# Performance work log

Measured on AMD Instinct MI355X. Metric: run time of the kernel, lower is better.

The kernel has to match this reference:

```python
import jax, jax.numpy as jnp
import numpy as np
import math

D_MODEL = 1024
D_HIDDEN = 64
H = 16
B = 2
N = 2048


def softmax_one(x, axis=-1):
    # exp(x - max) / (1 + sum(exp(x - max))) -- matches the torch code exactly
    m = jnp.max(x, axis=axis, keepdims=True)
    e = jnp.exp(x - m)
    return e / (1.0 + jnp.sum(e, axis=axis, keepdims=True))


def setup_inputs() -> dict:
    key = jax.random.key(0)
    ks = jax.random.split(key, 8)
    queries = jax.random.normal(ks[0], (B, N, D_MODEL), dtype=jnp.float32)
    keys = jax.random.normal(ks[1], (B, N, D_MODEL), dtype=jnp.float32)
    values = jax.random.normal(ks[2], (B, N, D_MODEL), dtype=jnp.float32)
    std = 0.02
    Wq = std * jax.random.normal(ks[3], (H * D_HIDDEN, D_MODEL), dtype=jnp.float32)
    Wk = std * jax.random.normal(ks[4], (H * D_HIDDEN, D_MODEL), dtype=jnp.float32)
    Wv = std * jax.random.normal(ks[5], (H * D_HIDDEN, D_MODEL), dtype=jnp.float32)
    Wo = std * jax.random.normal(ks[6], (D_MODEL, H * D_HIDDEN), dtype=jnp.float32)
    bq = jnp.zeros((H * D_HIDDEN,), jnp.float32)
    bk = jnp.zeros((H * D_HIDDEN,), jnp.float32)
    bv = jnp.zeros((H * D_HIDDEN,), jnp.float32)
    bo = jnp.zeros((D_MODEL,), jnp.float32)
    return {"queries": queries, "keys": keys, "values": values,
            "Wq": Wq, "bq": bq, "Wk": Wk, "bk": bk,
            "Wv": Wv, "bv": bv, "Wo": Wo, "bo": bo}


def reference(queries, keys, values, Wq, bq, Wk, bk, Wv, bv, Wo, bo):
    b_s, nq, _ = queries.shape
    nk = keys.shape[1]
    # projections: (b, n, h*dh) -> (b, h, n, dh)
    q = (queries @ Wq.T + bq).reshape(b_s, nq, H, D_HIDDEN).transpose(0, 2, 1, 3)
    k = (keys @ Wk.T + bk).reshape(b_s, nk, H, D_HIDDEN).transpose(0, 2, 1, 3)
    v = (values @ Wv.T + bv).reshape(b_s, nk, H, D_HIDDEN).transpose(0, 2, 1, 3)
    scale = 1.0 / math.sqrt(D_HIDDEN)
    scores = jnp.einsum('bhqd,bhkd->bhqk', q, k) * scale  # (b, h, nq, nk)
    attn = softmax_one(scores, axis=-1)  # dropout disabled (eval)
    out = jnp.einsum('bhqk,bhkd->bhqd', attn, v)  # (b, h, nq, dh)
    out = out.transpose(0, 2, 1, 3).reshape(b_s, nq, H * D_HIDDEN)
    out = out @ Wo.T + bo
    present = jnp.stack((k, v))  # (2, b, h, nk, dh)
    return (out, present)
```

## Files before the change

kernel.cpp:

```cpp
#include <hip/hip_runtime.h>
#include <math.h>

#define D_MODEL 1024
#define DH 64
#define NH 16
#define BS 2
#define SEQ 2048
#define MTOT (BS*SEQ)

typedef _Float16 f16x8 __attribute__((ext_vector_type(8)));
typedef _Float16 f16x4 __attribute__((ext_vector_type(4)));
typedef float f32x4 __attribute__((ext_vector_type(4)));
typedef unsigned int u32;

__device__ __forceinline__ void load_lds16(const void* g, void* l) {
    __builtin_amdgcn_global_load_lds(
        (const __attribute__((address_space(1))) u32*)g,
        (__attribute__((address_space(3))) u32*)l, 16, 0, 0);
}

__global__ __launch_bounds__(256) void convert_all_kernel(
    const float* __restrict__ s0, const float* __restrict__ s1, const float* __restrict__ s2,
    const float* __restrict__ s3, const float* __restrict__ s4, const float* __restrict__ s5,
    const float* __restrict__ s6,
    _Float16* __restrict__ d0, _Float16* __restrict__ d1, _Float16* __restrict__ d2,
    _Float16* __restrict__ d3, _Float16* __restrict__ d4, _Float16* __restrict__ d5,
    _Float16* __restrict__ d6, int nX, int nW)
{
    int y = blockIdx.y;
    const float* s; _Float16* d; int n;
    switch (y) {
        case 0: s = s0; d = d0; n = nX; break;
        case 1: s = s1; d = d1; n = nX; break;
        case 2: s = s2; d = d2; n = nX; break;
        case 3: s = s3; d = d3; n = nW; break;
        case 4: s = s4; d = d4; n = nW; break;
        case 5: s = s5; d = d5; n = nW; break;
        default: s = s6; d = d6; n = nW; break;
    }
    int i = (blockIdx.x * 256 + threadIdx.x) * 8;
    if (i < n) {
        float4 a = *(const float4*)(s + i);
        float4 b = *(const float4*)(s + i + 4);
        f16x8 o;
        o[0] = (_Float16)a.x; o[1] = (_Float16)a.y; o[2] = (_Float16)a.z; o[3] = (_Float16)a.w;
        o[4] = (_Float16)b.x; o[5] = (_Float16)b.y; o[6] = (_Float16)b.z; o[7] = (_Float16)b.w;
        *(f16x8*)(d + i) = o;
    }
}

__global__ __launch_bounds__(256) void qkv_proj_kernel(
    const _Float16* __restrict__ Xq, const _Float16* __restrict__ Xk, const _Float16* __restrict__ Xv,
    const _Float16* __restrict__ Wq, const _Float16* __restrict__ Wk, const _Float16* __restrict__ Wv,
    const float* __restrict__ bq, const float* __restrict__ bk, const float* __restrict__ bv,
    _Float16* __restrict__ qh, _Float16* __restrict__ kh, _Float16* __restrict__ vt,
    float* __restrict__ outp)
{
    __shared__ __align__(16) _Float16 ldsA[128][32];
    __shared__ __align__(16) _Float16 ldsB[128][32];

    const int jb = blockIdx.x >> 5;
    const int ib = blockIdx.x & 31;
    const int id = jb >> 3;
    const int col0 = (jb & 7) << 7;
    const int row0 = ib << 7;

    const _Float16* X  = (id == 0) ? Xq : (id == 1) ? Xk : Xv;
    const _Float16* W  = (id == 0) ? Wq : (id == 1) ? Wk : Wv;
    const float* bias  = (id == 0) ? bq : (id == 1) ? bk : bv;

    const int tid = threadIdx.x;
    const int w = tid >> 6, lane = tid & 63;
    const int quad = lane >> 4, l16 = lane & 15;
    const int wm = (w >> 1) << 6, wn = (w & 1) << 6;

    const int srow = w * 16 + (lane >> 2);
    const int scol = (lane & 3) << 3;

    const f32x4 zero = {0.f, 0.f, 0.f, 0.f};
    f32x4 acc[4][4];
#pragma unroll
    for (int i = 0; i < 4; i++)
#pragma unroll
        for (int j = 0; j < 4; j++) acc[i][j] = zero;

    for (int k0 = 0; k0 < D_MODEL; k0 += 32) {
        __syncthreads();
#pragma unroll
        for (int i = 0; i < 2; i++) {
            int r = i * 64 + srow;
            load_lds16(X + (size_t)(row0 + r) * D_MODEL + k0 + scol, &ldsA[i * 64 + w * 16][0]);
            load_lds16(W + (size_t)(col0 + r) * D_MODEL + k0 + scol, &ldsB[i * 64 + w * 16][0]);
        }
        __syncthreads();
        f16x8 af[4], bfr[4];
#pragma unroll
        for (int mi = 0; mi < 4; mi++) af[mi]  = *(const f16x8*)&ldsA[wm + mi*16 + l16][quad*8];
#pragma unroll
        for (int ni = 0; ni < 4; ni++) bfr[ni] = *(const f16x8*)&ldsB[wn + ni*16 + l16][quad*8];
#pragma unroll
        for (int mi = 0; mi < 4; mi++)
#pragma unroll
            for (int ni = 0; ni < 4; ni++)
                acc[mi][ni] = __builtin_amdgcn_mfma_f32_16x16x32_f16(af[mi], bfr[ni], acc[mi][ni], 0, 0, 0);
    }

    const size_t OUT0 = (size_t)MTOT * D_MODEL;
    const size_t PRES = (size_t)BS * NH * SEQ * DH;
#pragma unroll
    for (int ni = 0; ni < 4; ni++) {
        int gn = col0 + wn + ni * 16 + l16;
        float bias_v = bias[gn];
        int h = gn >> 6, d = gn & 63;
#pragma unroll
        for (int mi = 0; mi < 4; mi++) {
#pragma unroll
            for (int r = 0; r < 4; r++) {
                int gm = row0 + wm + mi * 16 + quad * 4 + r;
                float val = acc[mi][ni][r] + bias_v;
                int b = gm >> 11, n = gm & 2047;
                size_t bh = (size_t)(b * NH + h);
                size_t idx = (bh * SEQ + n) * DH + d;
                if (id == 0) {
                    qh[idx] = (_Float16)val;
                } else if (id == 1) {
                    outp[OUT0 + idx] = val;
                    kh[idx] = (_Float16)val;
                } else {
                    outp[OUT0 + PRES + idx] = val;
                    vt[(bh * DH + d) * SEQ + n] = (_Float16)val;
                }
            }
        }
    }
}

__global__ __launch_bounds__(256) void attn_kernel(
    const _Float16* __restrict__ qh, const _Float16* __restrict__ kh,
    const _Float16* __restrict__ vt, _Float16* __restrict__ aout)
{
    __shared__ __align__(16) _Float16 Kt[2][64][76];
    __shared__ __align__(16) _Float16 Vt[2][64][76];

    const int bh = blockIdx.x & 31;
    const int qt = blockIdx.x >> 5;
    const int b = bh >> 4, h = bh & 15;
    const int tid = threadIdx.x;
    const int w = tid >> 6, lane = tid & 63;
    const int quad = lane >> 4, l16 = lane & 15;
    const int qr0 = qt * 64 + w * 16;

    const _Float16* Qb = qh + (size_t)bh * SEQ * DH;
    const _Float16* Kb = kh + (size_t)bh * SEQ * DH;
    const _Float16* Vb = vt + (size_t)bh * DH * SEQ;

    const float QSCALE = 0.125f * 1.44269504f;
    f16x8 aq[2];
#pragma unroll
    for (int ks = 0; ks < 2; ks++) {
        f16x8 t = *(const f16x8*)(Qb + (size_t)(qr0 + l16) * DH + ks * 32 + quad * 8);
#pragma unroll
        for (int j = 0; j < 8; j++) t[j] = (_Float16)((float)t[j] * QSCALE);
        aq[ks] = t;
    }

    const int sr0 = tid >> 3, sc = (tid & 7) << 3;
    const int sr1 = sr0 + 32;

    {
        *(f16x8*)&Kt[0][sr0][sc] = *(const f16x8*)(Kb + (size_t)sr0 * DH + sc);
        *(f16x8*)&Kt[0][sr1][sc] = *(const f16x8*)(Kb + (size_t)sr1 * DH + sc);
        *(f16x8*)&Vt[0][sr0][sc] = *(const f16x8*)(Vb + (size_t)sr0 * SEQ + sc);
        *(f16x8*)&Vt[0][sr1][sc] = *(const f16x8*)(Vb + (size_t)sr1 * SEQ + sc);
    }
    __syncthreads();

    float m2 = -INFINITY, lsum = 0.f;
    const f32x4 zero = {0.f, 0.f, 0.f, 0.f};
    f32x4 accO[4];
#pragma unroll
    for (int db = 0; db < 4; db++) accO[db] = zero;

    for (int t = 0; t < SEQ / 64; t++) {
        const int cur = t & 1;
        const int kc = t * 64;

        f16x8 kr0, kr1, vr0, vr1;
        if (t + 1 < SEQ / 64) {
            const _Float16* kp = Kb + (size_t)(kc + 64) * DH;
            const _Float16* vp = Vb + kc + 64;
            kr0 = *(const f16x8*)(kp + (size_t)sr0 * DH + sc);
            kr1 = *(const f16x8*)(kp + (size_t)sr1 * DH + sc);
            vr0 = *(const f16x8*)(vp + (size_t)sr0 * SEQ + sc);
            vr1 = *(const f16x8*)(vp + (size_t)sr1 * SEQ + sc);
        }

        f32x4 sT[4];
#pragma unroll
        for (int nb = 0; nb < 4; nb++) sT[nb] = zero;
#pragma unroll
        for (int ks = 0; ks < 2; ks++)
#pragma unroll
            for (int nb = 0; nb < 4; nb++) {
                f16x8 kf = *(const f16x8*)&Kt[cur][nb*16 + l16][ks*32 + quad*8];
                sT[nb] = __builtin_amdgcn_mfma_f32_16x16x32_f16(kf, aq[ks], sT[nb], 0, 0, 0);
            }

        float smax = -INFINITY;
#pragma unroll
        for (int nb = 0; nb < 4; nb++)
#pragma unroll
            for (int r = 0; r < 4; r++) smax = fmaxf(smax, sT[nb][r]);
        smax = fmaxf(smax, __shfl_xor(smax, 16));
        smax = fmaxf(smax, __shfl_xor(smax, 32));
        float m2new = fmaxf(m2, smax);
        float alpha = __builtin_amdgcn_exp2f(m2 - m2new);

        float tsum = 0.f;
#pragma unroll
        for (int nb = 0; nb < 4; nb++)
#pragma unroll
            for (int r = 0; r < 4; r++) {
                float e = __builtin_amdgcn_exp2f(sT[nb][r] - m2new);
                sT[nb][r] = e;
                tsum += e;
            }
        tsum += __shfl_xor(tsum, 16);
        tsum += __shfl_xor(tsum, 32);
        lsum = lsum * alpha + tsum;
        m2 = m2new;

#pragma unroll
        for (int db = 0; db < 4; db++)
#pragma unroll
            for (int r = 0; r < 4; r++) accO[db][r] *= alpha;

        f16x4 pf[4];
#pragma unroll
        for (int nb = 0; nb < 4; nb++)
#pragma unroll
            for (int r = 0; r < 4; r++) pf[nb][r] = (_Float16)sT[nb][r];

#pragma unroll
        for (int db = 0; db < 4; db++)
#pragma unroll
            for (int nb = 0; nb < 4; nb++) {
                f16x4 vf = *(const f16x4*)&Vt[cur][db*16 + l16][nb*16 + quad*4];
                accO[db] = __builtin_amdgcn_mfma_f32_16x16x16f16(vf, pf[nb], accO[db], 0, 0, 0);
            }

        if (t + 1 < SEQ / 64) {
            *(f16x8*)&Kt[cur ^ 1][sr0][sc] = kr0;
            *(f16x8*)&Kt[cur ^ 1][sr1][sc] = kr1;
            *(f16x8*)&Vt[cur ^ 1][sr0][sc] = vr0;
            *(f16x8*)&Vt[cur ^ 1][sr1][sc] = vr1;
        }
        __syncthreads();
    }

    const float inv = 1.f / (1.f + lsum);
    const int q = qr0 + l16;
    _Float16* orow = aout + ((size_t)b * SEQ + q) * D_MODEL + h * DH + quad * 4;
#pragma unroll
    for (int db = 0; db < 4; db++) {
        f16x4 o;
#pragma unroll
        for (int r = 0; r < 4; r++) o[r] = (_Float16)(accO[db][r] * inv);
        *(f16x4*)(orow + db * 16) = o;
    }
}

__global__ __launch_bounds__(256) void out_proj_kernel(
    const _Float16* __restrict__ aout, const _Float16* __restrict__ Wo,
    const float* __restrict__ bo, float* __restrict__ outp)
{
    __shared__ __align__(16) _Float16 ldsA[128][32];
    __shared__ __align__(16) _Float16 ldsB[128][32];

    const int jb = blockIdx.x >> 5;
    const int ib = blockIdx.x & 31;
    const int col0 = jb << 7, row0 = ib << 7;
    const int tid = threadIdx.x;
    const int w = tid >> 6, lane = tid & 63;
    const int quad = lane >> 4, l16 = lane & 15;
    const int wm = (w >> 1) << 6, wn = (w & 1) << 6;

    const int srow = w * 16 + (lane >> 2);
    const int scol = (lane & 3) << 3;

    const f32x4 zero = {0.f, 0.f, 0.f, 0.f};
    f32x4 acc[4][4];
#pragma unroll
    for (int i = 0; i < 4; i++)
#pragma unroll
        for (int j = 0; j < 4; j++) acc[i][j] = zero;

    for (int k0 = 0; k0 < D_MODEL; k0 += 32) {
        __syncthreads();
#pragma unroll
        for (int i = 0; i < 2; i++) {
            int r = i * 64 + srow;
            load_lds16(aout + (size_t)(row0 + r) * D_MODEL + k0 + scol, &ldsA[i * 64 + w * 16][0]);
            load_lds16(Wo   + (size_t)(col0 + r) * D_MODEL + k0 + scol, &ldsB[i * 64 + w * 16][0]);
        }
        __syncthreads();
        f16x8 af[4], bfr[4];
#pragma unroll
        for (int mi = 0; mi < 4; mi++) af[mi]  = *(const f16x8*)&ldsA[wm + mi*16 + l16][quad*8];
#pragma unroll
        for (int ni = 0; ni < 4; ni++) bfr[ni] = *(const f16x8*)&ldsB[wn + ni*16 + l16][quad*8];
#pragma unroll
        for (int mi = 0; mi < 4; mi++)
#pragma unroll
            for (int ni = 0; ni < 4; ni++)
                acc[mi][ni] = __builtin_amdgcn_mfma_f32_16x16x32_f16(af[mi], bfr[ni], acc[mi][ni], 0, 0, 0);
    }

#pragma unroll
    for (int ni = 0; ni < 4; ni++) {
        int gn = col0 + wn + ni * 16 + l16;
        float bias_v = bo[gn];
#pragma unroll
        for (int mi = 0; mi < 4; mi++)
#pragma unroll
            for (int r = 0; r < 4; r++) {
                int gm = row0 + wm + mi * 16 + quad * 4 + r;
                outp[(size_t)gm * D_MODEL + gn] = acc[mi][ni][r] + bias_v;
            }
    }
}

extern "C" void kernel_launch(void* const* d_in, const int* in_sizes, int n_in,
                              void* d_out, int out_size, void* d_ws, size_t ws_size,
                              hipStream_t stream)
{
    const float* queries = (const float*)d_in[0];
    const float* keys    = (const float*)d_in[1];
    const float* values  = (const float*)d_in[2];
    const float* Wq = (const float*)d_in[3];
    const float* bq = (const float*)d_in[4];
    const float* Wk = (const float*)d_in[5];
    const float* bk = (const float*)d_in[6];
    const float* Wv = (const float*)d_in[7];
    const float* bv = (const float*)d_in[8];
    const float* Wo = (const float*)d_in[9];
    const float* bo = (const float*)d_in[10];
    float* outp = (float*)d_out;

    const size_t NELT = (size_t)BS * NH * SEQ * DH;
    const size_t XN   = (size_t)MTOT * D_MODEL;
    const size_t WN   = (size_t)D_MODEL * D_MODEL;
    _Float16* qh   = (_Float16*)d_ws;
    _Float16* kh   = qh + NELT;
    _Float16* vt   = kh + NELT;
    _Float16* aout = vt + NELT;
    _Float16* Xfq  = aout + NELT;
    _Float16* Xfk  = Xfq + XN;
    _Float16* Xfv  = Xfk + XN;
    _Float16* Wfq  = Xfv + XN;
    _Float16* Wfk  = Wfq + WN;
    _Float16* Wfv  = Wfk + WN;
    _Float16* Wfo  = Wfv + WN;

    convert_all_kernel<<<dim3((int)(XN/2048), 7), dim3(256), 0, stream>>>(
        queries, keys, values, Wq, Wk, Wv, Wo,
        Xfq, Xfk, Xfv, Wfq, Wfk, Wfv, Wfo, (int)XN, (int)WN);

    qkv_proj_kernel<<<dim3(768), dim3(256), 0, stream>>>(
        Xfq, Xfk, Xfv, Wfq, Wfk, Wfv, bq, bk, bv, qh, kh, vt, outp);
    attn_kernel<<<dim3(1024), dim3(256), 0, stream>>>(qh, kh, vt, aout);
    out_proj_kernel<<<dim3(256), dim3(256), 0, stream>>>(aout, Wfo, bo, outp);
}
```

Measured before the change: 265.3 us.

## Widen GEMM K-tiles with swizzled LDS, add V transpose kernel, enlarge attention blocks

The QKV and output projection GEMMs now stage 64-wide K slices per barrier and use an XOR-swizzled LDS layout, which halves the number of sync points and avoids bank conflicts. The output projection uses 64x128 tiles to launch more blocks. The scattered transposed V write in the projection epilogue is replaced by a separate kernel that rebuilds vt from the fp32 present output. Attention now runs 512-thread blocks covering 128 queries, so each K/V tile is shared by twice as many queries. The cost is an extra launch and a re-read of V in fp32.

```diff
diff --git a/kernel.cpp b/kernel.cpp
--- a/kernel.cpp
+++ b/kernel.cpp
@@ -53,11 +53,11 @@
     const _Float16* __restrict__ Xq, const _Float16* __restrict__ Xk, const _Float16* __restrict__ Xv,
     const _Float16* __restrict__ Wq, const _Float16* __restrict__ Wk, const _Float16* __restrict__ Wv,
     const float* __restrict__ bq, const float* __restrict__ bk, const float* __restrict__ bv,
-    _Float16* __restrict__ qh, _Float16* __restrict__ kh, _Float16* __restrict__ vt,
+    _Float16* __restrict__ qh, _Float16* __restrict__ kh,
     float* __restrict__ outp)
 {
-    __shared__ __align__(16) _Float16 ldsA[128][32];
-    __shared__ __align__(16) _Float16 ldsB[128][32];
+    __shared__ __align__(16) _Float16 ldsA[128][64];
+    __shared__ __align__(16) _Float16 ldsB[128][64];
 
     const int jb = blockIdx.x >> 5;
     const int ib = blockIdx.x & 31;
@@ -74,8 +74,8 @@
     const int quad = lane >> 4, l16 = lane & 15;
     const int wm = (w >> 1) << 6, wn = (w & 1) << 6;
 
-    const int srow = w * 16 + (lane >> 2);
-    const int scol = (lane & 3) << 3;
+    const int r_loc = lane >> 3;
+    const int sg = ((lane & 7) ^ r_loc) << 3;
 
     const f32x4 zero = {0.f, 0.f, 0.f, 0.f};
     f32x4 acc[4][4];
@@ -84,25 +84,30 @@
 #pragma unroll
         for (int j = 0; j < 4; j++) acc[i][j] = zero;
 
-    for (int k0 = 0; k0 < D_MODEL; k0 += 32) {
-        __syncthreads();
-#pragma unroll
-        for (int i = 0; i < 2; i++) {
-            int r = i * 64 + srow;
-            load_lds16(X + (size_t)(row0 + r) * D_MODEL + k0 + scol, &ldsA[i * 64 + w * 16][0]);
-            load_lds16(W + (size_t)(col0 + r) * D_MODEL + k0 + scol, &ldsB[i * 64 + w * 16][0]);
-        }
-        __syncthreads();
-        f16x8 af[4], bfr[4];
-#pragma unroll
-        for (int mi = 0; mi < 4; mi++) af[mi]  = *(const f16x8*)&ldsA[wm + mi*16 + l16][quad*8];
-#pragma unroll
-        for (int ni = 0; ni < 4; ni++) bfr[ni] = *(const f16x8*)&ldsB[wn + ni*16 + l16][quad*8];
-#pragma unroll
-        for (int mi = 0; mi < 4; mi++)
+    for (int k0 = 0; k0 < D_MODEL; k0 += 64) {
+        __syncthreads();
+#pragma unroll
+        for (int i = 0; i < 4; i++) {
+            int r = i * 32 + w * 8 + r_loc;
+            load_lds16(X + (size_t)(row0 + r) * D_MODEL + k0 + sg, &ldsA[i * 32 + w * 8][0]);
+            load_lds16(W + (size_t)(col0 + r) * D_MODEL + k0 + sg, &ldsB[i * 32 + w * 8][0]);
+        }
+        __syncthreads();
+#pragma unroll
+        for (int kk = 0; kk < 2; kk++) {
+            f16x8 af[4], bfr[4];
+#pragma unroll
+            for (int mi = 0; mi < 4; mi++)
+                af[mi]  = *(const f16x8*)&ldsA[wm + mi*16 + l16][(((kk<<2) + quad) ^ (l16 & 7)) << 3];
 #pragma unroll
             for (int ni = 0; ni < 4; ni++)
-                acc[mi][ni] = __builtin_amdgcn_mfma_f32_16x16x32_f16(af[mi], bfr[ni], acc[mi][ni], 0, 0, 0);
+                bfr[ni] = *(const f16x8*)&ldsB[wn + ni*16 + l16][(((kk<<2) + quad) ^ (l16 & 7)) << 3];
+#pragma unroll
+            for (int mi = 0; mi < 4; mi++)
+#pragma unroll
+                for (int ni = 0; ni < 4; ni++)
+                    acc[mi][ni] = __builtin_amdgcn_mfma_f32_16x16x32_f16(af[mi], bfr[ni], acc[mi][ni], 0, 0, 0);
+        }
     }
 
     const size_t OUT0 = (size_t)MTOT * D_MODEL;
@@ -128,14 +133,27 @@
                     kh[idx] = (_Float16)val;
                 } else {
                     outp[OUT0 + PRES + idx] = val;
-                    vt[(bh * DH + d) * SEQ + n] = (_Float16)val;
                 }
             }
         }
     }
 }
 
-__global__ __launch_bounds__(256) void attn_kernel(
+__global__ __launch_bounds__(256) void vtrans_kernel(
+    const float* __restrict__ p1, _Float16* __restrict__ vt)
+{
+    const int bh = blockIdx.x >> 6, nt = blockIdx.x & 63;
+    const int tid = threadIdx.x;
+    const int d = tid & 63, n8 = tid >> 6;
+    const int n0 = nt * 32 + n8 * 8;
+    const float* src = p1 + ((size_t)bh * SEQ + n0) * DH + d;
+    f16x8 o;
+#pragma unroll
+    for (int i = 0; i < 8; i++) o[i] = (_Float16)src[(size_t)i * DH];
+    *(f16x8*)(vt + ((size_t)bh * DH + d) * SEQ + n0) = o;
+}
+
+__global__ __launch_bounds__(512) void attn_kernel(
     const _Float16* __restrict__ qh, const _Float16* __restrict__ kh,
     const _Float16* __restrict__ vt, _Float16* __restrict__ aout)
 {
@@ -148,7 +166,7 @@
     const int tid = threadIdx.x;
     const int w = tid >> 6, lane = tid & 63;
     const int quad = lane >> 4, l16 = lane & 15;
-    const int qr0 = qt * 64 + w * 16;
+    const int qr0 = qt * 128 + w * 16;
 
     const _Float16* Qb = qh + (size_t)bh * SEQ * DH;
     const _Float16* Kb = kh + (size_t)bh * SEQ * DH;
@@ -164,15 +182,10 @@
         aq[ks] = t;
     }
 
-    const int sr0 = tid >> 3, sc = (tid & 7) << 3;
-    const int sr1 = sr0 + 32;
-
-    {
-        *(f16x8*)&Kt[0][sr0][sc] = *(const f16x8*)(Kb + (size_t)sr0 * DH + sc);
-        *(f16x8*)&Kt[0][sr1][sc] = *(const f16x8*)(Kb + (size_t)sr1 * DH + sc);
-        *(f16x8*)&Vt[0][sr0][sc] = *(const f16x8*)(Vb + (size_t)sr0 * SEQ + sc);
-        *(f16x8*)&Vt[0][sr1][sc] = *(const f16x8*)(Vb + (size_t)sr1 * SEQ + sc);
-    }
+    const int sr = tid >> 3, sc = (tid & 7) << 3;
+
+    *(f16x8*)&Kt[0][sr][sc] = *(const f16x8*)(Kb + (size_t)sr * DH + sc);
+    *(f16x8*)&Vt[0][sr][sc] = *(const f16x8*)(Vb + (size_t)sr * SEQ + sc);
     __syncthreads();
 
     float m2 = -INFINITY, lsum = 0.f;
@@ -185,14 +198,10 @@
         const int cur = t & 1;
         const int kc = t * 64;
 
-        f16x8 kr0, kr1, vr0, vr1;
+        f16x8 kr, vr;
         if (t + 1 < SEQ / 64) {
-            const _Float16* kp = Kb + (size_t)(kc + 64) * DH;
-            const _Float16* vp = Vb + kc + 64;
-            kr0 = *(const f16x8*)(kp + (size_t)sr0 * DH + sc);
-            kr1 = *(const f16x8*)(kp + (size_t)sr1 * DH + sc);
-            vr0 = *(const f16x8*)(vp + (size_t)sr0 * SEQ + sc);
-            vr1 = *(const f16x8*)(vp + (size_t)sr1 * SEQ + sc);
+            kr = *(const f16x8*)(Kb + (size_t)(kc + 64 + sr) * DH + sc);
+            vr = *(const f16x8*)(Vb + (size_t)sr * SEQ + kc + 64 + sc);
         }
 
         f32x4 sT[4];
@@ -250,10 +259,8 @@
             }
 
         if (t + 1 < SEQ / 64) {
-            *(f16x8*)&Kt[cur ^ 1][sr0][sc] = kr0;
-            *(f16x8*)&Kt[cur ^ 1][sr1][sc] = kr1;
-            *(f16x8*)&Vt[cur ^ 1][sr0][sc] = vr0;
-            *(f16x8*)&Vt[cur ^ 1][sr1][sc] = vr1;
+            *(f16x8*)&Kt[cur ^ 1][sr][sc] = kr;
+            *(f16x8*)&Vt[cur ^ 1][sr][sc] = vr;
         }
         __syncthreads();
     }
@@ -274,46 +281,55 @@
     const _Float16* __restrict__ aout, const _Float16* __restrict__ Wo,
     const float* __restrict__ bo, float* __restrict__ outp)
 {
-    __shared__ __align__(16) _Float16 ldsA[128][32];
-    __shared__ __align__(16) _Float16 ldsB[128][32];
-
-    const int jb = blockIdx.x >> 5;
-    const int ib = blockIdx.x & 31;
-    const int col0 = jb << 7, row0 = ib << 7;
+    __shared__ __align__(16) _Float16 ldsA[64][64];
+    __shared__ __align__(16) _Float16 ldsB[128][64];
+
+    const int jb = blockIdx.x >> 6;
+    const int ib = blockIdx.x & 63;
+    const int col0 = jb << 7, row0 = ib << 6;
     const int tid = threadIdx.x;
     const int w = tid >> 6, lane = tid & 63;
     const int quad = lane >> 4, l16 = lane & 15;
-    const int wm = (w >> 1) << 6, wn = (w & 1) << 6;
-
-    const int srow = w * 16 + (lane >> 2);
-    const int scol = (lane & 3) << 3;
+    const int wm = (w >> 1) << 5, wn = (w & 1) << 6;
+
+    const int r_loc = lane >> 3;
+    const int sg = ((lane & 7) ^ r_loc) << 3;
 
     const f32x4 zero = {0.f, 0.f, 0.f, 0.f};
-    f32x4 acc[4][4];
-#pragma unroll
-    for (int i = 0; i < 4; i++)
+    f32x4 acc[2][4];
+#pragma unroll
+    for (int i = 0; i < 2; i++)
 #pragma unroll
         for (int j = 0; j < 4; j++) acc[i][j] = zero;
 
-    for (int k0 = 0; k0 < D_MODEL; k0 += 32) {
+    for (int k0 = 0; k0 < D_MODEL; k0 += 64) {
         __syncthreads();
 #pragma unroll
         for (int i = 0; i < 2; i++) {
-            int r = i * 64 + srow;
-            load_lds16(aout + (size_t)(row0 + r) * D_MODEL + k0 + scol, &ldsA[i * 64 + w * 16][0]);
-            load_lds16(Wo   + (size_t)(col0 + r) * D_MODEL + k0 + scol, &ldsB[i * 64 + w * 16][0]);
-        }
-        __syncthreads();
-        f16x8 af[4], bfr[4];
-#pragma unroll
-        for (int mi = 0; mi < 4; mi++) af[mi]  = *(const f16x8*)&ldsA[wm + mi*16 + l16][quad*8];
-#pragma unroll
-        for (int ni = 0; ni < 4; ni++) bfr[ni] = *(const f16x8*)&ldsB[wn + ni*16 + l16][quad*8];
-#pragma unroll
-        for (int mi = 0; mi < 4; mi++)
+            int r = i * 32 + w * 8 + r_loc;
+            load_lds16(aout + (size_t)(row0 + r) * D_MODEL + k0 + sg, &ldsA[i * 32 + w * 8][0]);
+        }
+#pragma unroll
+        for (int i = 0; i < 4; i++) {
+            int r = i * 32 + w * 8 + r_loc;
+            load_lds16(Wo + (size_t)(col0 + r) * D_MODEL + k0 + sg, &ldsB[i * 32 + w * 8][0]);
+        }
+        __syncthreads();
+#pragma unroll
+        for (int kk = 0; kk < 2; kk++) {
+            f16x8 af[2], bfr[4];
+#pragma unroll
+            for (int mi = 0; mi < 2; mi++)
+                af[mi]  = *(const f16x8*)&ldsA[wm + mi*16 + l16][(((kk<<2) + quad) ^ (l16 & 7)) << 3];
 #pragma unroll
             for (int ni = 0; ni < 4; ni++)
-                acc[mi][ni] = __builtin_amdgcn_mfma_f32_16x16x32_f16(af[mi], bfr[ni], acc[mi][ni], 0, 0, 0);
+                bfr[ni] = *(const f16x8*)&ldsB[wn + ni*16 + l16][(((kk<<2) + quad) ^ (l16 & 7)) << 3];
+#pragma unroll
+            for (int mi = 0; mi < 2; mi++)
+#pragma unroll
+                for (int ni = 0; ni < 4; ni++)
+                    acc[mi][ni] = __builtin_amdgcn_mfma_f32_16x16x32_f16(af[mi], bfr[ni], acc[mi][ni], 0, 0, 0);
+        }
     }
 
 #pragma unroll
@@ -321,7 +337,7 @@
         int gn = col0 + wn + ni * 16 + l16;
         float bias_v = bo[gn];
 #pragma unroll
-        for (int mi = 0; mi < 4; mi++)
+        for (int mi = 0; mi < 2; mi++)
 #pragma unroll
             for (int r = 0; r < 4; r++) {
                 int gm = row0 + wm + mi * 16 + quad * 4 + r;
@@ -362,12 +378,17 @@
     _Float16* Wfv  = Wfk + WN;
     _Float16* Wfo  = Wfv + WN;
 
+    const size_t OUT0 = (size_t)MTOT * D_MODEL;
+    const size_t PRES = NELT;
+    const float* present1 = outp + OUT0 + PRES;
+
     convert_all_kernel<<<dim3((int)(XN/2048), 7), dim3(256), 0, stream>>>(
         queries, keys, values, Wq, Wk, Wv, Wo,
         Xfq, Xfk, Xfv, Wfq, Wfk, Wfv, Wfo, (int)XN, (int)WN);
 
     qkv_proj_kernel<<<dim3(768), dim3(256), 0, stream>>>(
-        Xfq, Xfk, Xfv, Wfq, Wfk, Wfv, bq, bk, bv, qh, kh, vt, outp);
-    attn_kernel<<<dim3(1024), dim3(256), 0, stream>>>(qh, kh, vt, aout);
-    out_proj_kernel<<<dim3(256), dim3(256), 0, stream>>>(aout, Wfo, bo, outp);
-}
+        Xfq, Xfk, Xfv, Wfq, Wfk, Wfv, bq, bk, bv, qh, kh, outp);
+    vtrans_kernel<<<dim3(2048), dim3(256), 0, stream>>>(present1, vt);
+    attn_kernel<<<dim3(512), dim3(512), 0, stream>>>(qh, kh, vt, aout);
+    out_proj_kernel<<<dim3(512), dim3(256), 0, stream>>>(aout, Wfo, bo, outp);
+}
```

Result: faster. 253.5 us (-4.4%).
